# Kernel tuning notes

Hardware: AMD Instinct MI355X
Metric: run time of the kernel (lower is better)

## Reference

```python
import jax, jax.numpy as jnp
import numpy as np

BN_EPS = 1e-5

def _bn(h, g, b, m, v):
    # eval-mode BatchNorm1d with running stats
    return g * (h - m) * jax.lax.rsqrt(v + BN_EPS) + b

def setup_inputs() -> dict:
    key = jax.random.key(0)
    ks = jax.random.split(key, 16)
    N, E, F, H, P, C, L = 100000, 1600000, 128, 128, 128, 10, 3
    s = 0.05
    return {
        "x": jax.random.normal(ks[0], (N, F), jnp.float32),
        "edge_index": jax.random.randint(ks[1], (2, E), 0, N, jnp.int64),
        "eps": jnp.zeros((L,), jnp.float32),
        "W1": jax.random.normal(ks[2], (L, F, H), jnp.float32) * s,
        "b1": jax.random.normal(ks[3], (L, H), jnp.float32) * s,
        "bn1_g": jax.random.uniform(ks[4], (L, H), jnp.float32, 0.5, 1.5),
        "bn1_b": jax.random.normal(ks[5], (L, H), jnp.float32) * s,
        "bn1_m": jnp.zeros((L, H), jnp.float32),
        "bn1_v": jnp.ones((L, H), jnp.float32),
        "W2": jax.random.normal(ks[6], (L, H, H), jnp.float32) * s,
        "b2": jax.random.normal(ks[7], (L, H), jnp.float32) * s,
        "bn2_g": jax.random.uniform(ks[8], (L, H), jnp.float32, 0.5, 1.5),
        "bn2_b": jax.random.normal(ks[9], (L, H), jnp.float32) * s,
        "bn2_m": jnp.zeros((L, H), jnp.float32),
        "bn2_v": jnp.ones((L, H), jnp.float32),
        "lin1_W": jax.random.normal(ks[10], (H, P), jnp.float32) * s,
        "lin1_b": jax.random.normal(ks[11], (P,), jnp.float32) * s,
        "lin2_W": jax.random.normal(ks[12], (P, C), jnp.float32) * s,
        "lin2_b": jax.random.normal(ks[13], (C,), jnp.float32) * s,
    }

def reference(x, edge_index, eps, W1, b1, bn1_g, bn1_b, bn1_m, bn1_v,
              W2, b2, bn2_g, bn2_b, bn2_m, bn2_v,
              lin1_W, lin1_b, lin2_W, lin2_b):
    N = x.shape[0]
    L = W1.shape[0]
    src, dst = edge_index[0], edge_index[1]
    for i in range(L):
        # GINConv: sum-aggregate neighbor features, add (1+eps)*self
        agg = jax.ops.segment_sum(x[src], dst, num_segments=N)  # [N, F]
        h = (1.0 + eps[i]) * x + agg
        h = jax.nn.relu(_bn(h @ W1[i] + b1[i], bn1_g[i], bn1_b[i], bn1_m[i], bn1_v[i]))
        h = jax.nn.relu(_bn(h @ W2[i] + b2[i], bn2_g[i], bn2_b[i], bn2_m[i], bn2_v[i]))
        x = jax.nn.relu(h)  # outer F.relu in GIN.forward (no-op after ReLU, kept for fidelity)
    h = jax.nn.relu(x @ lin1_W + lin1_b)
    logits = h @ lin2_W + lin2_b
    return jax.nn.log_softmax(logits, axis=-1)
```

## Files before the change

### kernel.cpp

```cpp
#include <hip/hip_runtime.h>
#include <hip/hip_fp16.h>


#define PB 256
#define MAXNB 512

typedef _Float16 f16x8 __attribute__((ext_vector_type(8)));
typedef float f32x4 __attribute__((ext_vector_type(4)));

struct H4 { __half2 a, b; };

__global__ void detect_idx_kernel(const unsigned int* __restrict__ w, long long nOdd,
                                  int* __restrict__ flag) {
    __shared__ int any;
    if (threadIdx.x == 0) any = 0;
    __syncthreads();
    for (long long i = threadIdx.x; i < nOdd; i += blockDim.x) {
        if (w[2 * i + 1] != 0u) { any = 1; break; }
    }
    __syncthreads();
    if (threadIdx.x == 0) *flag = (any == 0) ? 1 : 0;
}

__global__ __launch_bounds__(256) void p1_hist_kernel(
    const void* __restrict__ idx, long long E, const int* __restrict__ flag,
    int* __restrict__ cnt_mat, int NB) {
    __shared__ int h[MAXNB];
    for (int i = threadIdx.x; i < MAXNB; i += 256) h[i] = 0;
    __syncthreads();
    const long long C = (E + PB - 1) / PB;
    const long long lo = (long long)blockIdx.x * C;
    long long hi = lo + C; if (hi > E) hi = E;
    if (*flag) {
        const long long* pd = (const long long*)idx + E;
        for (long long i = lo + threadIdx.x; i < hi; i += 256)
            atomicAdd(&h[((int)pd[i]) >> 8], 1);
    } else {
        const int* pd = (const int*)idx + E;
        for (long long i = lo + threadIdx.x; i < hi; i += 256)
            atomicAdd(&h[pd[i] >> 8], 1);
    }
    __syncthreads();
    for (int i = threadIdx.x; i < NB; i += 256)
        cnt_mat[i * PB + blockIdx.x] = h[i];
}

__global__ __launch_bounds__(256) void scan_bucket_kernel(
    int* __restrict__ cnt_mat, int* __restrict__ btotal) {
    int k = blockIdx.x, t = threadIdx.x;
    __shared__ int sh[PB];
    int c = cnt_mat[k * PB + t];
    sh[t] = c;
    __syncthreads();
    for (int off = 1; off < PB; off <<= 1) {
        int v = (t >= off) ? sh[t - off] : 0;
        __syncthreads();
        sh[t] += v;
        __syncthreads();
    }
    cnt_mat[k * PB + t] = sh[t] - c;
    if (t == PB - 1) btotal[k] = sh[t];
}

__global__ __launch_bounds__(512) void scan_btotal_kernel(
    const int* __restrict__ btotal, int* __restrict__ bbase, int* __restrict__ boff,
    int NB, int N, long long E, int* __restrict__ row_ptr) {
    int t = threadIdx.x;
    __shared__ int sh[512];
    int c = (t < NB) ? btotal[t] : 0;
    sh[t] = c;
    __syncthreads();
    for (int off = 1; off < 512; off <<= 1) {
        int v = (t >= off) ? sh[t - off] : 0;
        __syncthreads();
        sh[t] += v;
        __syncthreads();
    }
    int excl = sh[t] - c;
    if (t < NB) { bbase[t] = excl; boff[t] = excl; }
    if (t == 0) { boff[NB] = (int)E; row_ptr[N] = (int)E; }
}

__global__ __launch_bounds__(256) void p2_scatter_kernel(
    const void* __restrict__ idx, long long E, const int* __restrict__ flag,
    const int* __restrict__ cnt_mat, const int* __restrict__ bbase,
    uint2* __restrict__ bdata, int NB) {
    __shared__ int cur[MAXNB];
    int b = blockIdx.x;
    for (int i = threadIdx.x; i < NB; i += 256)
        cur[i] = cnt_mat[i * PB + b] + bbase[i];
    __syncthreads();
    const long long C = (E + PB - 1) / PB;
    const long long lo = (long long)b * C;
    long long hi = lo + C; if (hi > E) hi = E;
    if (*flag) {
        const long long* ps = (const long long*)idx;
        const long long* pd = ps + E;
        for (long long i = lo + threadIdx.x; i < hi; i += 256) {
            int s = (int)ps[i], d = (int)pd[i];
            int r = atomicAdd(&cur[d >> 8], 1);
            bdata[r] = make_uint2((unsigned)s, (unsigned)d);
        }
    } else {
        const int* ps = (const int*)idx;
        const int* pd = ps + E;
        for (long long i = lo + threadIdx.x; i < hi; i += 256) {
            int s = ps[i], d = pd[i];
            int r = atomicAdd(&cur[d >> 8], 1);
            bdata[r] = make_uint2((unsigned)s, (unsigned)d);
        }
    }
}

__global__ __launch_bounds__(256) void csr_build_kernel(
    const uint2* __restrict__ bdata, const int* __restrict__ boff, int N,
    int* __restrict__ row_ptr, int* __restrict__ csr_src) {
    int b = blockIdx.x, t = threadIdx.x;
    int lo = boff[b], hi = boff[b + 1];
    int nb = b << 8;
    __shared__ int cnt[256];
    __shared__ int sh[256];
    cnt[t] = 0;
    __syncthreads();
    for (int i = lo + t; i < hi; i += 256)
        atomicAdd(&cnt[bdata[i].y & 255], 1);
    __syncthreads();
    int c = cnt[t];
    sh[t] = c;
    __syncthreads();
    for (int off = 1; off < 256; off <<= 1) {
        int v = (t >= off) ? sh[t - off] : 0;
        __syncthreads();
        sh[t] += v;
        __syncthreads();
    }
    int excl = sh[t] - c;
    if (nb + t < N) row_ptr[nb + t] = lo + excl;
    cnt[t] = excl;
    __syncthreads();
    for (int i = lo + t; i < hi; i += 256) {
        uint2 e = bdata[i];
        int p = atomicAdd(&cnt[e.y & 255], 1);
        csr_src[lo + p] = (int)e.x;
    }
}

__global__ void convert_x_kernel(__half* __restrict__ out, const float* __restrict__ in,
                                 int n4) {
    int i = blockIdx.x * blockDim.x + threadIdx.x;
    int stride = gridDim.x * blockDim.x;
    const float4* in4 = (const float4*)in;
    for (; i < n4; i += stride) {
        float4 v = in4[i];
        H4 h;
        h.a = __float22half2_rn(make_float2(v.x, v.y));
        h.b = __float22half2_rn(make_float2(v.z, v.w));
        *(H4*)(out + i * 4) = h;
    }
}

__global__ void pack_w_kernel(__half* __restrict__ pk, const float* __restrict__ W1,
                              const float* __restrict__ W2, const float* __restrict__ lin1) {
    int t = blockIdx.x * blockDim.x + threadIdx.x;
    if (t >= 7 * 2048) return;
    int mat = t >> 11;
    int rem = t & 2047;
    int ks = rem >> 9;
    int ct = (rem >> 6) & 7;
    int lane = rem & 63;
    int g = lane >> 4, c = lane & 15;
    const float* src = (mat < 3) ? W1 + mat * 16384
                     : (mat < 6) ? W2 + (mat - 3) * 16384
                                 : lin1;
    __half* dst = pk + mat * 16384 + ((size_t)((ks * 8 + ct) * 64 + lane)) * 8;
#pragma unroll
    for (int j = 0; j < 8; ++j)
        dst[j] = (__half)src[(ks * 32 + g * 8 + j) * 128 + ct * 16 + c];
}

__global__ __launch_bounds__(256) void gather_h_kernel(
    __half* __restrict__ out, const __half* __restrict__ x,
    const int* __restrict__ row_ptr, const int* __restrict__ csr,
    const float* __restrict__ eps, int layer, int N) {
    int wave = threadIdx.x >> 6;
    int lane = threadIdx.x & 63;
    int g = lane >> 4;
    int t = lane & 15;
    int wid = blockIdx.x * 4 + wave;
    int nw = gridDim.x * 4;
    float s = 1.0f + eps[layer];
    for (int n = wid; n < N; n += nw) {
        int beg = row_ptr[n], end = row_ptr[n + 1];
        float2 a0 = make_float2(0.f, 0.f), a1 = a0, a2 = a0, a3 = a0;
#define ACC16(vv) { \
        float2 f0 = __half22float2(((const __half2*)&(vv))[0]); \
        float2 f1 = __half22float2(((const __half2*)&(vv))[1]); \
        float2 f2 = __half22float2(((const __half2*)&(vv))[2]); \
        float2 f3 = __half22float2(((const __half2*)&(vv))[3]); \
        a0.x += f0.x; a0.y += f0.y; a1.x += f1.x; a1.y += f1.y; \
        a2.x += f2.x; a2.y += f2.y; a3.x += f3.x; a3.y += f3.y; }
        int j = beg + g;
        for (; j + 4 < end; j += 8) {
            uint4 v0 = *(const uint4*)(x + (long long)csr[j] * 128 + t * 8);
            uint4 v1 = *(const uint4*)(x + (long long)csr[j + 4] * 128 + t * 8);
            ACC16(v0);
            ACC16(v1);
        }
        if (j < end) {
            uint4 v0 = *(const uint4*)(x + (long long)csr[j] * 128 + t * 8);
            ACC16(v0);
        }
#undef ACC16
        a0.x += __shfl_xor(a0.x, 16); a0.y += __shfl_xor(a0.y, 16);
        a1.x += __shfl_xor(a1.x, 16); a1.y += __shfl_xor(a1.y, 16);
        a2.x += __shfl_xor(a2.x, 16); a2.y += __shfl_xor(a2.y, 16);
        a3.x += __shfl_xor(a3.x, 16); a3.y += __shfl_xor(a3.y, 16);
        a0.x += __shfl_xor(a0.x, 32); a0.y += __shfl_xor(a0.y, 32);
        a1.x += __shfl_xor(a1.x, 32); a1.y += __shfl_xor(a1.y, 32);
        a2.x += __shfl_xor(a2.x, 32); a2.y += __shfl_xor(a2.y, 32);
        a3.x += __shfl_xor(a3.x, 32); a3.y += __shfl_xor(a3.y, 32);
        if (g == 0) {
            uint4 sv = *(const uint4*)(x + (long long)n * 128 + t * 8);
            float2 f0 = __half22float2(((const __half2*)&sv)[0]);
            float2 f1 = __half22float2(((const __half2*)&sv)[1]);
            float2 f2 = __half22float2(((const __half2*)&sv)[2]);
            float2 f3 = __half22float2(((const __half2*)&sv)[3]);
            a0.x = fmaf(s, f0.x, a0.x); a0.y = fmaf(s, f0.y, a0.y);
            a1.x = fmaf(s, f1.x, a1.x); a1.y = fmaf(s, f1.y, a1.y);
            a2.x = fmaf(s, f2.x, a2.x); a2.y = fmaf(s, f2.y, a2.y);
            a3.x = fmaf(s, f3.x, a3.x); a3.y = fmaf(s, f3.y, a3.y);
            uint4 o;
            ((__half2*)&o)[0] = __float22half2_rn(a0);
            ((__half2*)&o)[1] = __float22half2_rn(a1);
            ((__half2*)&o)[2] = __float22half2_rn(a2);
            ((__half2*)&o)[3] = __float22half2_rn(a3);
            *(uint4*)(out + (long long)n * 128 + t * 8) = o;
        }
    }
}

__global__ __launch_bounds__(256) void gemm12_h_kernel(
    const __half* __restrict__ in,
    const __half* __restrict__ pk1, const float* __restrict__ b1,
    const float* __restrict__ g1, const float* __restrict__ bb1,
    const float* __restrict__ m1, const float* __restrict__ v1,
    const __half* __restrict__ pk2, const float* __restrict__ b2,
    const float* __restrict__ g2, const float* __restrict__ bb2,
    const float* __restrict__ m2, const float* __restrict__ v2,
    __half* __restrict__ out, int N) {
    __shared__ __half sA[128 * 128];
    __shared__ float sc1_s[128], sh1_s[128], sc2_s[128], sh2_s[128];

    const int tid = threadIdx.x;
    if (tid < 128) {
        int c = tid;
        float sc = g1[c] * rsqrtf(v1[c] + 1e-5f);
        sc1_s[c] = sc;
        sh1_s[c] = b1[c] * sc + bb1[c] - m1[c] * sc;
        sc = g2[c] * rsqrtf(v2[c] + 1e-5f);
        sc2_s[c] = sc;
        sh2_s[c] = b2[c] * sc + bb2[c] - m2[c] * sc;
    }

    const int base = blockIdx.x * 128;
#pragma unroll
    for (int q = 0; q < 8; ++q) {
        int i = tid + q * 256;
        int row = i >> 4, c = i & 15;
        int r = base + row;
        if (r >= N) r = N - 1;
        uint4 v = *(const uint4*)(in + r * 128 + c * 8);
        *(uint4*)&sA[row * 128 + ((c ^ (row & 15)) * 8)] = v;
    }
    __syncthreads();

    const int wave = tid >> 6;
    const int lane = tid & 63;
    const int g16 = lane >> 4;
    const int r15 = lane & 15;

    f32x4 acc[2][8];
#pragma unroll
    for (int rt = 0; rt < 2; ++rt)
#pragma unroll
        for (int ct = 0; ct < 8; ++ct) acc[rt][ct] = (f32x4)0.f;

#pragma unroll
    for (int ks = 0; ks < 4; ++ks) {
        f16x8 wf[8];
#pragma unroll
        for (int ct = 0; ct < 8; ++ct)
            wf[ct] = *(const f16x8*)(pk1 + ((ks * 8 + ct) * 64 + lane) * 8);
#pragma unroll
        for (int rt = 0; rt < 2; ++rt) {
            int row = wave * 32 + rt * 16 + r15;
            f16x8 bf = *(const f16x8*)&sA[row * 128 + (((ks * 4 + g16) ^ r15) * 8)];
#pragma unroll
            for (int ct = 0; ct < 8; ++ct)
                acc[rt][ct] = __builtin_amdgcn_mfma_f32_16x16x32_f16(wf[ct], bf,
                                                                     acc[rt][ct], 0, 0, 0);
        }
    }

    __syncthreads();
#pragma unroll
    for (int rt = 0; rt < 2; ++rt) {
        int row = wave * 32 + rt * 16 + r15;
#pragma unroll
        for (int ct = 0; ct < 8; ++ct) {
            int col = ct * 16 + g16 * 4;
            float4 sc4 = *(float4*)&sc1_s[col];
            float4 sh4 = *(float4*)&sh1_s[col];
            f32x4 a = acc[rt][ct];
            float o0 = fmaxf(fmaf(a[0], sc4.x, sh4.x), 0.f);
            float o1 = fmaxf(fmaf(a[1], sc4.y, sh4.y), 0.f);
            float o2 = fmaxf(fmaf(a[2], sc4.z, sh4.z), 0.f);
            float o3 = fmaxf(fmaf(a[3], sc4.w, sh4.w), 0.f);
            H4 h;
            h.a = __float22half2_rn(make_float2(o0, o1));
            h.b = __float22half2_rn(make_float2(o2, o3));
            int c = col >> 3;
            *(H4*)&sA[row * 128 + ((c ^ (row & 15)) * 8) + (col & 7)] = h;
        }
    }
    __syncthreads();

#pragma unroll
    for (int rt = 0; rt < 2; ++rt)
#pragma unroll
        for (int ct = 0; ct < 8; ++ct) acc[rt][ct] = (f32x4)0.f;
#pragma unroll
    for (int ks = 0; ks < 4; ++ks) {
        f16x8 wf[8];
#pragma unroll
        for (int ct = 0; ct < 8; ++ct)
            wf[ct] = *(const f16x8*)(pk2 + ((ks * 8 + ct) * 64 + lane) * 8);
#pragma unroll
        for (int rt = 0; rt < 2; ++rt) {
            int row = wave * 32 + rt * 16 + r15;
            f16x8 bf = *(const f16x8*)&sA[row * 128 + (((ks * 4 + g16) ^ r15) * 8)];
#pragma unroll
            for (int ct = 0; ct < 8; ++ct)
                acc[rt][ct] = __builtin_amdgcn_mfma_f32_16x16x32_f16(wf[ct], bf,
                                                                     acc[rt][ct], 0, 0, 0);
        }
    }

#pragma unroll
    for (int rt = 0; rt < 2; ++rt) {
        int r = base + wave * 32 + rt * 16 + r15;
        if (r < N) {
            __half* orow = out + r * 128;
#pragma unroll
            for (int ct = 0; ct < 8; ++ct) {
                int col = ct * 16 + g16 * 4;
                float4 sc4 = *(float4*)&sc2_s[col];
                float4 sh4 = *(float4*)&sh2_s[col];
                f32x4 a = acc[rt][ct];
                float o0 = fmaxf(fmaf(a[0], sc4.x, sh4.x), 0.f);
                float o1 = fmaxf(fmaf(a[1], sc4.y, sh4.y), 0.f);
                float o2 = fmaxf(fmaf(a[2], sc4.z, sh4.z), 0.f);
                float o3 = fmaxf(fmaf(a[3], sc4.w, sh4.w), 0.f);
                H4 h;
                h.a = __float22half2_rn(make_float2(o0, o1));
                h.b = __float22half2_rn(make_float2(o2, o3));
                *(H4*)(orow + col) = h;
            }
        }
    }
}

__global__ __launch_bounds__(256) void lin1_head_kernel(
    const __half* __restrict__ in, const __half* __restrict__ pk1,
    const float* __restrict__ l1b, const float* __restrict__ l2W,
    const float* __restrict__ l2b, float* __restrict__ out, int N) {
    __shared__ __half sA[128 * 128];
    __shared__ float Wl[1280];
    __shared__ float bl[10];
    __shared__ float b1_s[128];

    const int tid = threadIdx.x;
    for (int i = tid; i < 1280; i += 256) Wl[i] = l2W[i];
    if (tid < 10) bl[tid] = l2b[tid];
    if (tid < 128) b1_s[tid] = l1b[tid];

    const int base = blockIdx.x * 128;
#pragma unroll
    for (int q = 0; q < 8; ++q) {
        int i = tid + q * 256;
        int row = i >> 4, c = i & 15;
        int r = base + row;
        if (r >= N) r = N - 1;
        uint4 v = *(const uint4*)(in + r * 128 + c * 8);
        *(uint4*)&sA[row * 128 + ((c ^ (row & 15)) * 8)] = v;
    }
    __syncthreads();

    const int wave = tid >> 6;
    const int lane = tid & 63;
    const int g16 = lane >> 4;
    const int r15 = lane & 15;

    f32x4 acc[2][8];
#pragma unroll
    for (int rt = 0; rt < 2; ++rt)
#pragma unroll
        for (int ct = 0; ct < 8; ++ct) acc[rt][ct] = (f32x4)0.f;

#pragma unroll
    for (int ks = 0; ks < 4; ++ks) {
        f16x8 wf[8];
#pragma unroll
        for (int ct = 0; ct < 8; ++ct)
            wf[ct] = *(const f16x8*)(pk1 + ((ks * 8 + ct) * 64 + lane) * 8);
#pragma unroll
        for (int rt = 0; rt < 2; ++rt) {
            int row = wave * 32 + rt * 16 + r15;
            f16x8 bf = *(const f16x8*)&sA[row * 128 + (((ks * 4 + g16) ^ r15) * 8)];
#pragma unroll
            for (int ct = 0; ct < 8; ++ct)
                acc[rt][ct] = __builtin_amdgcn_mfma_f32_16x16x32_f16(wf[ct], bf,
                                                                     acc[rt][ct], 0, 0, 0);
        }
    }

#pragma unroll
    for (int rt = 0; rt < 2; ++rt) {
        float p[10];
#pragma unroll
        for (int c = 0; c < 10; ++c) p[c] = 0.f;
#pragma unroll
        for (int ct = 0; ct < 8; ++ct) {
            int col0 = ct * 16 + g16 * 4;
#pragma unroll
            for (int j = 0; j < 4; ++j) {
                int col = col0 + j;
                float h = fmaxf(acc[rt][ct][j] + b1_s[col], 0.f);
#pragma unroll
                for (int c = 0; c < 10; ++c) p[c] = fmaf(h, Wl[col * 10 + c], p[c]);
            }
        }
#pragma unroll
        for (int c = 0; c < 10; ++c) {
            p[c] += __shfl_xor(p[c], 16);
            p[c] += __shfl_xor(p[c], 32);
        }
        int r = base + wave * 32 + rt * 16 + r15;
        if (g16 == 0 && r < N) {
            float mx = -1e30f;
#pragma unroll
            for (int c = 0; c < 10; ++c) {
                p[c] += bl[c];
                mx = fmaxf(mx, p[c]);
            }
            float sum = 0.f;
#pragma unroll
            for (int c = 0; c < 10; ++c) sum += expf(p[c] - mx);
            float lse = mx + logf(sum);
            float* orow = out + (long long)r * 10;
#pragma unroll
            for (int c = 0; c < 10; ++c) orow[c] = p[c] - lse;
        }
    }
}

extern "C" void kernel_launch(void* const* d_in, const int* in_sizes, int n_in,
                              void* d_out, int out_size, void* d_ws, size_t ws_size,
                              hipStream_t stream) {
    const float* x   = (const float*)d_in[0];
    const void*  eix = d_in[1];
    const float* eps = (const float*)d_in[2];
    const float* W1  = (const float*)d_in[3];
    const float* b1  = (const float*)d_in[4];
    const float* g1  = (const float*)d_in[5];
    const float* bb1 = (const float*)d_in[6];
    const float* m1  = (const float*)d_in[7];
    const float* v1  = (const float*)d_in[8];
    const float* W2  = (const float*)d_in[9];
    const float* b2  = (const float*)d_in[10];
    const float* g2  = (const float*)d_in[11];
    const float* bb2 = (const float*)d_in[12];
    const float* m2  = (const float*)d_in[13];
    const float* v2  = (const float*)d_in[14];
    const float* l1W = (const float*)d_in[15];
    const float* l1b = (const float*)d_in[16];
    const float* l2W = (const float*)d_in[17];
    const float* l2b = (const float*)d_in[18];

    const int N = in_sizes[0] / 128;
    const long long E = in_sizes[1] / 2;
    const int NB = (N + 255) >> 8;

    __half* bufA  = (__half*)d_ws;
    __half* bufB  = bufA + (size_t)N * 128;
    __half* pk    = bufB + (size_t)N * 128;
    uint2*  bdata = (uint2*)(pk + 7 * 16384);
    int* csr_src  = (int*)(bdata + E);
    int* row_ptr  = csr_src + E;
    int* cnt_mat  = row_ptr + N + 1;
    int* btotal   = cnt_mat + MAXNB * PB;
    int* bbase    = btotal + MAXNB;
    int* boff     = bbase + MAXNB;
    int* flag     = boff + MAXNB + 1;

    detect_idx_kernel<<<1, 256, 0, stream>>>((const unsigned int*)eix,
                                             (E < 2048 ? E : 2048), flag);

    p1_hist_kernel<<<PB, 256, 0, stream>>>(eix, E, flag, cnt_mat, NB);
    scan_bucket_kernel<<<NB, 256, 0, stream>>>(cnt_mat, btotal);
    scan_btotal_kernel<<<1, 512, 0, stream>>>(btotal, bbase, boff, NB, N, E, row_ptr);
    p2_scatter_kernel<<<PB, 256, 0, stream>>>(eix, E, flag, cnt_mat, bbase, bdata, NB);
    csr_build_kernel<<<NB, 256, 0, stream>>>(bdata, boff, N, row_ptr, csr_src);

    convert_x_kernel<<<2048, 256, 0, stream>>>(bufA, x, N * 32);
    pack_w_kernel<<<(7 * 2048 + 255) / 256, 256, 0, stream>>>(pk, W1, W2, l1W);

    const int gBlocks = 2048;
    const int mBlocks = (N + 127) / 128;

    __half* cur = bufA;
    __half* oth = bufB;
    for (int l = 0; l < 3; ++l) {
        gather_h_kernel<<<gBlocks, 256, 0, stream>>>(oth, cur, row_ptr, csr_src, eps, l, N);
        gemm12_h_kernel<<<mBlocks, 256, 0, stream>>>(
            oth,
            pk + (size_t)l * 16384, b1 + l * 128, g1 + l * 128, bb1 + l * 128,
            m1 + l * 128, v1 + l * 128,
            pk + (size_t)(3 + l) * 16384, b2 + l * 128, g2 + l * 128, bb2 + l * 128,
            m2 + l * 128, v2 + l * 128,
            oth, N);
        __half* t = cur; cur = oth; oth = t;
    }
    lin1_head_kernel<<<mBlocks, 256, 0, stream>>>(
        cur, pk + (size_t)6 * 16384, l1b, l2W, l2b, (float*)d_out, N);
}
```

Baseline: 338.2 us.

## Fuse neighbor gather into GEMM kernel, writing aggregated rows to shared memory

Merges the per-layer CSR gather kernel into the two-GEMM MLP kernel. Each block now aggregates neighbors for its own 128 rows, with each wave handling 32 rows, and writes the fp16 results straight into the swizzled shared-memory A tile. This removes one kernel launch per layer and the global-memory write and reread of the aggregated features. In exchange, gather parallelism is tied to the GEMM grid of 128-row blocks, and the 32KB shared-memory tile may lower occupancy during the latency-bound gather phase.

```diff
diff --git a/kernel.cpp b/kernel.cpp
--- a/kernel.cpp
+++ b/kernel.cpp
@@ -178,19 +178,42 @@
         dst[j] = (__half)src[(ks * 32 + g * 8 + j) * 128 + ct * 16 + c];
 }
 
-__global__ __launch_bounds__(256) void gather_h_kernel(
-    __half* __restrict__ out, const __half* __restrict__ x,
-    const int* __restrict__ row_ptr, const int* __restrict__ csr,
-    const float* __restrict__ eps, int layer, int N) {
-    int wave = threadIdx.x >> 6;
-    int lane = threadIdx.x & 63;
-    int g = lane >> 4;
-    int t = lane & 15;
-    int wid = blockIdx.x * 4 + wave;
-    int nw = gridDim.x * 4;
-    float s = 1.0f + eps[layer];
-    for (int n = wid; n < N; n += nw) {
-        int beg = row_ptr[n], end = row_ptr[n + 1];
+__global__ __launch_bounds__(256) void gin_layer_kernel(
+    const __half* __restrict__ in, const int* __restrict__ row_ptr,
+    const int* __restrict__ csr, const float* __restrict__ eps, int layer,
+    const __half* __restrict__ pk1, const float* __restrict__ b1,
+    const float* __restrict__ g1, const float* __restrict__ bb1,
+    const float* __restrict__ m1, const float* __restrict__ v1,
+    const __half* __restrict__ pk2, const float* __restrict__ b2,
+    const float* __restrict__ g2, const float* __restrict__ bb2,
+    const float* __restrict__ m2, const float* __restrict__ v2,
+    __half* __restrict__ out, int N) {
+    __shared__ __half sA[128 * 128];
+    __shared__ float sc1_s[128], sh1_s[128], sc2_s[128], sh2_s[128];
+
+    const int tid = threadIdx.x;
+    if (tid < 128) {
+        int c = tid;
+        float sc = g1[c] * rsqrtf(v1[c] + 1e-5f);
+        sc1_s[c] = sc;
+        sh1_s[c] = b1[c] * sc + bb1[c] - m1[c] * sc;
+        sc = g2[c] * rsqrtf(v2[c] + 1e-5f);
+        sc2_s[c] = sc;
+        sh2_s[c] = b2[c] * sc + bb2[c] - m2[c] * sc;
+    }
+
+    const int base = blockIdx.x * 128;
+    const int wave = tid >> 6;
+    const int lane = tid & 63;
+    const int g = lane >> 4;
+    const int t = lane & 15;
+    const float s = 1.0f + eps[layer];
+
+    for (int k = 0; k < 32; ++k) {
+        int row = wave * 32 + k;
+        int r = base + row;
+        int rc = (r < N) ? r : (N - 1);
+        int beg = row_ptr[rc], end = row_ptr[rc + 1];
         float2 a0 = make_float2(0.f, 0.f), a1 = a0, a2 = a0, a3 = a0;
 #define ACC16(vv) { \
         float2 f0 = __half22float2(((const __half2*)&(vv))[0]); \
@@ -201,13 +224,13 @@
         a2.x += f2.x; a2.y += f2.y; a3.x += f3.x; a3.y += f3.y; }
         int j = beg + g;
         for (; j + 4 < end; j += 8) {
-            uint4 v0 = *(const uint4*)(x + (long long)csr[j] * 128 + t * 8);
-            uint4 v1 = *(const uint4*)(x + (long long)csr[j + 4] * 128 + t * 8);
+            uint4 v0 = *(const uint4*)(in + (long long)csr[j] * 128 + t * 8);
+            uint4 v1 = *(const uint4*)(in + (long long)csr[j + 4] * 128 + t * 8);
             ACC16(v0);
             ACC16(v1);
         }
         if (j < end) {
-            uint4 v0 = *(const uint4*)(x + (long long)csr[j] * 128 + t * 8);
+            uint4 v0 = *(const uint4*)(in + (long long)csr[j] * 128 + t * 8);
             ACC16(v0);
         }
 #undef ACC16
@@ -220,7 +243,7 @@
         a2.x += __shfl_xor(a2.x, 32); a2.y += __shfl_xor(a2.y, 32);
         a3.x += __shfl_xor(a3.x, 32); a3.y += __shfl_xor(a3.y, 32);
         if (g == 0) {
-            uint4 sv = *(const uint4*)(x + (long long)n * 128 + t * 8);
+            uint4 sv = *(const uint4*)(in + (long long)rc * 128 + t * 8);
             float2 f0 = __half22float2(((const __half2*)&sv)[0]);
             float2 f1 = __half22float2(((const __half2*)&sv)[1]);
             float2 f2 = __half22float2(((const __half2*)&sv)[2]);
@@ -234,48 +257,11 @@
             ((__half2*)&o)[1] = __float22half2_rn(a1);
             ((__half2*)&o)[2] = __float22half2_rn(a2);
             ((__half2*)&o)[3] = __float22half2_rn(a3);
-            *(uint4*)(out + (long long)n * 128 + t * 8) = o;
-        }
-    }
-}
-
-__global__ __launch_bounds__(256) void gemm12_h_kernel(
-    const __half* __restrict__ in,
-    const __half* __restrict__ pk1, const float* __restrict__ b1,
-    const float* __restrict__ g1, const float* __restrict__ bb1,
-    const float* __restrict__ m1, const float* __restrict__ v1,
-    const __half* __restrict__ pk2, const float* __restrict__ b2,
-    const float* __restrict__ g2, const float* __restrict__ bb2,
-    const float* __restrict__ m2, const float* __restrict__ v2,
-    __half* __restrict__ out, int N) {
-    __shared__ __half sA[128 * 128];
-    __shared__ float sc1_s[128], sh1_s[128], sc2_s[128], sh2_s[128];
-
-    const int tid = threadIdx.x;
-    if (tid < 128) {
-        int c = tid;
-        float sc = g1[c] * rsqrtf(v1[c] + 1e-5f);
-        sc1_s[c] = sc;
-        sh1_s[c] = b1[c] * sc + bb1[c] - m1[c] * sc;
-        sc = g2[c] * rsqrtf(v2[c] + 1e-5f);
-        sc2_s[c] = sc;
-        sh2_s[c] = b2[c] * sc + bb2[c] - m2[c] * sc;
-    }
-
-    const int base = blockIdx.x * 128;
-#pragma unroll
-    for (int q = 0; q < 8; ++q) {
-        int i = tid + q * 256;
-        int row = i >> 4, c = i & 15;
-        int r = base + row;
-        if (r >= N) r = N - 1;
-        uint4 v = *(const uint4*)(in + r * 128 + c * 8);
-        *(uint4*)&sA[row * 128 + ((c ^ (row & 15)) * 8)] = v;
-    }
-    __syncthreads();
-
-    const int wave = tid >> 6;
-    const int lane = tid & 63;
+            *(uint4*)&sA[row * 128 + ((t ^ (row & 15)) * 8)] = o;
+        }
+    }
+    __syncthreads();
+
     const int g16 = lane >> 4;
     const int r15 = lane & 15;
 
@@ -515,15 +501,13 @@
     convert_x_kernel<<<2048, 256, 0, stream>>>(bufA, x, N * 32);
     pack_w_kernel<<<(7 * 2048 + 255) / 256, 256, 0, stream>>>(pk, W1, W2, l1W);
 
-    const int gBlocks = 2048;
     const int mBlocks = (N + 127) / 128;
 
     __half* cur = bufA;
     __half* oth = bufB;
     for (int l = 0; l < 3; ++l) {
-        gather_h_kernel<<<gBlocks, 256, 0, stream>>>(oth, cur, row_ptr, csr_src, eps, l, N);
-        gemm12_h_kernel<<<mBlocks, 256, 0, stream>>>(
-            oth,
+        gin_layer_kernel<<<mBlocks, 256, 0, stream>>>(
+            cur, row_ptr, csr_src, eps, l,
             pk + (size_t)l * 16384, b1 + l * 128, g1 + l * 128, bb1 + l * 128,
             m1 + l * 128, v1 + l * 128,
             pk + (size_t)(3 + l) * 16384, b2 + l * 128, g2 + l * 128, bb2 + l * 128,
```

After: 652.2 us. +92.8%, slower.

## Fuse last GIN layer MLP with classifier head; pack CSR bucket entries

Applied to the files above, without the earlier changes.

The third layer's two-GEMM MLP is fused with the lin1/lin2/log-softmax head in one kernel. The intermediate activations stay in LDS instead of being written to and re-read from global memory, and one launch is removed. The bucket scatter data is also packed into a single 32-bit word (src<<8 | dst&255) instead of a uint2, which halves that buffer's traffic. The packing assumes node indices fit in 24 bits, and the fused kernel uses more shared memory, which may lower occupancy.

```diff
diff --git a/kernel.cpp b/kernel.cpp
--- a/kernel.cpp
+++ b/kernel.cpp
@@ -84,7 +84,7 @@
 __global__ __launch_bounds__(256) void p2_scatter_kernel(
     const void* __restrict__ idx, long long E, const int* __restrict__ flag,
     const int* __restrict__ cnt_mat, const int* __restrict__ bbase,
-    uint2* __restrict__ bdata, int NB) {
+    unsigned* __restrict__ bdata, int NB) {
     __shared__ int cur[MAXNB];
     int b = blockIdx.x;
     for (int i = threadIdx.x; i < NB; i += 256)
@@ -99,7 +99,7 @@
         for (long long i = lo + threadIdx.x; i < hi; i += 256) {
             int s = (int)ps[i], d = (int)pd[i];
             int r = atomicAdd(&cur[d >> 8], 1);
-            bdata[r] = make_uint2((unsigned)s, (unsigned)d);
+            bdata[r] = ((unsigned)s << 8) | (unsigned)(d & 255);
         }
     } else {
         const int* ps = (const int*)idx;
@@ -107,13 +107,13 @@
         for (long long i = lo + threadIdx.x; i < hi; i += 256) {
             int s = ps[i], d = pd[i];
             int r = atomicAdd(&cur[d >> 8], 1);
-            bdata[r] = make_uint2((unsigned)s, (unsigned)d);
+            bdata[r] = ((unsigned)s << 8) | (unsigned)(d & 255);
         }
     }
 }
 
 __global__ __launch_bounds__(256) void csr_build_kernel(
-    const uint2* __restrict__ bdata, const int* __restrict__ boff, int N,
+    const unsigned* __restrict__ bdata, const int* __restrict__ boff, int N,
     int* __restrict__ row_ptr, int* __restrict__ csr_src) {
     int b = blockIdx.x, t = threadIdx.x;
     int lo = boff[b], hi = boff[b + 1];
@@ -123,7 +123,7 @@
     cnt[t] = 0;
     __syncthreads();
     for (int i = lo + t; i < hi; i += 256)
-        atomicAdd(&cnt[bdata[i].y & 255], 1);
+        atomicAdd(&cnt[bdata[i] & 255], 1);
     __syncthreads();
     int c = cnt[t];
     sh[t] = c;
@@ -139,9 +139,9 @@
     cnt[t] = excl;
     __syncthreads();
     for (int i = lo + t; i < hi; i += 256) {
-        uint2 e = bdata[i];
-        int p = atomicAdd(&cnt[e.y & 255], 1);
-        csr_src[lo + p] = (int)e.x;
+        unsigned e = bdata[i];
+        int p = atomicAdd(&cnt[e & 255], 1);
+        csr_src[lo + p] = (int)(e >> 8);
     }
 }
 
@@ -239,6 +239,50 @@
     }
 }
 
+#define MFMA_GEMM(PK)                                                          \
+    _Pragma("unroll")                                                          \
+    for (int rt = 0; rt < 2; ++rt)                                             \
+        _Pragma("unroll")                                                      \
+        for (int ct = 0; ct < 8; ++ct) acc[rt][ct] = (f32x4)0.f;               \
+    _Pragma("unroll")                                                          \
+    for (int ks = 0; ks < 4; ++ks) {                                           \
+        f16x8 wf[8];                                                           \
+        _Pragma("unroll")                                                      \
+        for (int ct = 0; ct < 8; ++ct)                                         \
+            wf[ct] = *(const f16x8*)((PK) + ((ks * 8 + ct) * 64 + lane) * 8);  \
+        _Pragma("unroll")                                                      \
+        for (int rt = 0; rt < 2; ++rt) {                                       \
+            int row = wave * 32 + rt * 16 + r15;                               \
+            f16x8 bf = *(const f16x8*)&sA[row * 128 + (((ks * 4 + g16) ^ r15) * 8)]; \
+            _Pragma("unroll")                                                  \
+            for (int ct = 0; ct < 8; ++ct)                                     \
+                acc[rt][ct] = __builtin_amdgcn_mfma_f32_16x16x32_f16(wf[ct], bf, \
+                                                                     acc[rt][ct], 0, 0, 0); \
+        }                                                                      \
+    }
+
+#define EPI_TO_LDS(SC, SH)                                                     \
+    _Pragma("unroll")                                                          \
+    for (int rt = 0; rt < 2; ++rt) {                                           \
+        int row = wave * 32 + rt * 16 + r15;                                   \
+        _Pragma("unroll")                                                      \
+        for (int ct = 0; ct < 8; ++ct) {                                       \
+            int col = ct * 16 + g16 * 4;                                       \
+            float4 sc4 = *(float4*)&(SC)[col];                                 \
+            float4 sh4 = *(float4*)&(SH)[col];                                 \
+            f32x4 a = acc[rt][ct];                                             \
+            float o0 = fmaxf(fmaf(a[0], sc4.x, sh4.x), 0.f);                   \
+            float o1 = fmaxf(fmaf(a[1], sc4.y, sh4.y), 0.f);                   \
+            float o2 = fmaxf(fmaf(a[2], sc4.z, sh4.z), 0.f);                   \
+            float o3 = fmaxf(fmaf(a[3], sc4.w, sh4.w), 0.f);                   \
+            H4 h;                                                              \
+            h.a = __float22half2_rn(make_float2(o0, o1));                      \
+            h.b = __float22half2_rn(make_float2(o2, o3));                      \
+            int cc = col >> 3;                                                 \
+            *(H4*)&sA[row * 128 + ((cc ^ (row & 15)) * 8) + (col & 7)] = h;    \
+        }                                                                      \
+    }
+
 __global__ __launch_bounds__(256) void gemm12_h_kernel(
     const __half* __restrict__ in,
     const __half* __restrict__ pk1, const float* __restrict__ b1,
@@ -280,71 +324,11 @@
     const int r15 = lane & 15;
 
     f32x4 acc[2][8];
-#pragma unroll
-    for (int rt = 0; rt < 2; ++rt)
-#pragma unroll
-        for (int ct = 0; ct < 8; ++ct) acc[rt][ct] = (f32x4)0.f;
-
-#pragma unroll
-    for (int ks = 0; ks < 4; ++ks) {
-        f16x8 wf[8];
-#pragma unroll
-        for (int ct = 0; ct < 8; ++ct)
-            wf[ct] = *(const f16x8*)(pk1 + ((ks * 8 + ct) * 64 + lane) * 8);
-#pragma unroll
-        for (int rt = 0; rt < 2; ++rt) {
-            int row = wave * 32 + rt * 16 + r15;
-            f16x8 bf = *(const f16x8*)&sA[row * 128 + (((ks * 4 + g16) ^ r15) * 8)];
-#pragma unroll
-            for (int ct = 0; ct < 8; ++ct)
-                acc[rt][ct] = __builtin_amdgcn_mfma_f32_16x16x32_f16(wf[ct], bf,
-                                                                     acc[rt][ct], 0, 0, 0);
-        }
-    }
-
-    __syncthreads();
-#pragma unroll
-    for (int rt = 0; rt < 2; ++rt) {
-        int row = wave * 32 + rt * 16 + r15;
-#pragma unroll
-        for (int ct = 0; ct < 8; ++ct) {
-            int col = ct * 16 + g16 * 4;
-            float4 sc4 = *(float4*)&sc1_s[col];
-            float4 sh4 = *(float4*)&sh1_s[col];
-            f32x4 a = acc[rt][ct];
-            float o0 = fmaxf(fmaf(a[0], sc4.x, sh4.x), 0.f);
-            float o1 = fmaxf(fmaf(a[1], sc4.y, sh4.y), 0.f);
-            float o2 = fmaxf(fmaf(a[2], sc4.z, sh4.z), 0.f);
-            float o3 = fmaxf(fmaf(a[3], sc4.w, sh4.w), 0.f);
-            H4 h;
-            h.a = __float22half2_rn(make_float2(o0, o1));
-            h.b = __float22half2_rn(make_float2(o2, o3));
-            int c = col >> 3;
-            *(H4*)&sA[row * 128 + ((c ^ (row & 15)) * 8) + (col & 7)] = h;
-        }
-    }
-    __syncthreads();
-
-#pragma unroll
-    for (int rt = 0; rt < 2; ++rt)
-#pragma unroll
-        for (int ct = 0; ct < 8; ++ct) acc[rt][ct] = (f32x4)0.f;
-#pragma unroll
-    for (int ks = 0; ks < 4; ++ks) {
-        f16x8 wf[8];
-#pragma unroll
-        for (int ct = 0; ct < 8; ++ct)
-            wf[ct] = *(const f16x8*)(pk2 + ((ks * 8 + ct) * 64 + lane) * 8);
-#pragma unroll
-        for (int rt = 0; rt < 2; ++rt) {
-            int row = wave * 32 + rt * 16 + r15;
-            f16x8 bf = *(const f16x8*)&sA[row * 128 + (((ks * 4 + g16) ^ r15) * 8)];
-#pragma unroll
-            for (int ct = 0; ct < 8; ++ct)
-                acc[rt][ct] = __builtin_amdgcn_mfma_f32_16x16x32_f16(wf[ct], bf,
-                                                                     acc[rt][ct], 0, 0, 0);
-        }
-    }
+    MFMA_GEMM(pk1);
+    __syncthreads();
+    EPI_TO_LDS(sc1_s, sh1_s);
+    __syncthreads();
+    MFMA_GEMM(pk2);
 
 #pragma unroll
     for (int rt = 0; rt < 2; ++rt) {
@@ -370,19 +354,36 @@
     }
 }
 
-__global__ __launch_bounds__(256) void lin1_head_kernel(
-    const __half* __restrict__ in, const __half* __restrict__ pk1,
-    const float* __restrict__ l1b, const float* __restrict__ l2W,
-    const float* __restrict__ l2b, float* __restrict__ out, int N) {
+__global__ __launch_bounds__(256) void gemm12_head_kernel(
+    const __half* __restrict__ in,
+    const __half* __restrict__ pk1, const float* __restrict__ b1,
+    const float* __restrict__ g1, const float* __restrict__ bb1,
+    const float* __restrict__ m1, const float* __restrict__ v1,
+    const __half* __restrict__ pk2, const float* __restrict__ b2,
+    const float* __restrict__ g2, const float* __restrict__ bb2,
+    const float* __restrict__ m2, const float* __restrict__ v2,
+    const __half* __restrict__ pk3, const float* __restrict__ l1b,
+    const float* __restrict__ l2W, const float* __restrict__ l2b,
+    float* __restrict__ out, int N) {
     __shared__ __half sA[128 * 128];
+    __shared__ float sc1_s[128], sh1_s[128], sc2_s[128], sh2_s[128];
     __shared__ float Wl[1280];
     __shared__ float bl[10];
     __shared__ float b1_s[128];
 
     const int tid = threadIdx.x;
+    if (tid < 128) {
+        int c = tid;
+        float sc = g1[c] * rsqrtf(v1[c] + 1e-5f);
+        sc1_s[c] = sc;
+        sh1_s[c] = b1[c] * sc + bb1[c] - m1[c] * sc;
+        sc = g2[c] * rsqrtf(v2[c] + 1e-5f);
+        sc2_s[c] = sc;
+        sh2_s[c] = b2[c] * sc + bb2[c] - m2[c] * sc;
+        b1_s[c] = l1b[c];
+    }
     for (int i = tid; i < 1280; i += 256) Wl[i] = l2W[i];
     if (tid < 10) bl[tid] = l2b[tid];
-    if (tid < 128) b1_s[tid] = l1b[tid];
 
     const int base = blockIdx.x * 128;
 #pragma unroll
@@ -402,27 +403,15 @@
     const int r15 = lane & 15;
 
     f32x4 acc[2][8];
-#pragma unroll
-    for (int rt = 0; rt < 2; ++rt)
-#pragma unroll
-        for (int ct = 0; ct < 8; ++ct) acc[rt][ct] = (f32x4)0.f;
-
-#pragma unroll
-    for (int ks = 0; ks < 4; ++ks) {
-        f16x8 wf[8];
-#pragma unroll
-        for (int ct = 0; ct < 8; ++ct)
-            wf[ct] = *(const f16x8*)(pk1 + ((ks * 8 + ct) * 64 + lane) * 8);
-#pragma unroll
-        for (int rt = 0; rt < 2; ++rt) {
-            int row = wave * 32 + rt * 16 + r15;
-            f16x8 bf = *(const f16x8*)&sA[row * 128 + (((ks * 4 + g16) ^ r15) * 8)];
-#pragma unroll
-            for (int ct = 0; ct < 8; ++ct)
-                acc[rt][ct] = __builtin_amdgcn_mfma_f32_16x16x32_f16(wf[ct], bf,
-                                                                     acc[rt][ct], 0, 0, 0);
-        }
-    }
+    MFMA_GEMM(pk1);
+    __syncthreads();
+    EPI_TO_LDS(sc1_s, sh1_s);
+    __syncthreads();
+    MFMA_GEMM(pk2);
+    __syncthreads();
+    EPI_TO_LDS(sc2_s, sh2_s);
+    __syncthreads();
+    MFMA_GEMM(pk3);
 
 #pragma unroll
     for (int rt = 0; rt < 2; ++rt) {
@@ -494,7 +483,7 @@
     __half* bufA  = (__half*)d_ws;
     __half* bufB  = bufA + (size_t)N * 128;
     __half* pk    = bufB + (size_t)N * 128;
-    uint2*  bdata = (uint2*)(pk + 7 * 16384);
+    unsigned* bdata = (unsigned*)(pk + 7 * 16384);
     int* csr_src  = (int*)(bdata + E);
     int* row_ptr  = csr_src + E;
     int* cnt_mat  = row_ptr + N + 1;
@@ -520,7 +509,7 @@
 
     __half* cur = bufA;
     __half* oth = bufB;
-    for (int l = 0; l < 3; ++l) {
+    for (int l = 0; l < 2; ++l) {
         gather_h_kernel<<<gBlocks, 256, 0, stream>>>(oth, cur, row_ptr, csr_src, eps, l, N);
         gemm12_h_kernel<<<mBlocks, 256, 0, stream>>>(
             oth,
@@ -531,6 +520,13 @@
             oth, N);
         __half* t = cur; cur = oth; oth = t;
     }
-    lin1_head_kernel<<<mBlocks, 256, 0, stream>>>(
-        cur, pk + (size_t)6 * 16384, l1b, l2W, l2b, (float*)d_out, N);
-}
+    gather_h_kernel<<<gBlocks, 256, 0, stream>>>(oth, cur, row_ptr, csr_src, eps, 2, N);
+    gemm12_head_kernel<<<mBlocks, 256, 0, stream>>>(
+        oth,
+        pk + (size_t)2 * 16384, b1 + 2 * 128, g1 + 2 * 128, bb1 + 2 * 128,
+        m1 + 2 * 128, v1 + 2 * 128,
+        pk + (size_t)5 * 16384, b2 + 2 * 128, g2 + 2 * 128, bb2 + 2 * 128,
+        m2 + 2 * 128, v2 + 2 * 128,
+        pk + (size_t)6 * 16384, l1b, l2W, l2b,
+        (float*)d_out, N);
+}
```

After: 331.8 us. Within noise of the previous version (-1.9%).
